# Kernel optimization log

Hardware: AMD Instinct MI355X
Metric: run time of the kernel (lower is better)

The kernel has to match this reference:

```python
import jax, jax.numpy as jnp
import numpy as np

T = 2048        # flattened tokens (one prefill sequence)
HID = 2048      # hidden_size
NH = 32         # query heads
NKV = 4         # kv heads
HD = 128        # head_dim
THETA = 1000000.0
EPS = 1e-6


def setup_inputs() -> dict:
    key = jax.random.key(0)
    k0, k1, k2 = jax.random.split(key, 3)
    return {
        "positions": jnp.arange(T, dtype=jnp.int32),
        "hidden_states": jax.random.normal(k0, (T, HID), dtype=jnp.float32),
        "w_qkv": jax.random.normal(k1, ((NH + 2 * NKV) * HD, HID), dtype=jnp.float32) * 0.02,
        "w_o": jax.random.normal(k2, (HID, NH * HD), dtype=jnp.float32) * 0.02,
        "q_norm_w": jnp.ones((HD,), dtype=jnp.float32),
        "k_norm_w": jnp.ones((HD,), dtype=jnp.float32),
    }


def _rmsnorm(x, w):
    # per-head RMSNorm over last dim (head_dim), fp32 math
    var = jnp.mean(x * x, axis=-1, keepdims=True)
    return x * jax.lax.rsqrt(var + EPS) * w


def _rope(x, positions):
    # NeoX-style rotary embedding over full head_dim
    d = x.shape[-1]
    inv_freq = 1.0 / (THETA ** (jnp.arange(0, d, 2, dtype=jnp.float32) / d))  # [d/2]
    ang = positions.astype(jnp.float32)[:, None] * inv_freq                   # [T, d/2]
    cos = jnp.cos(ang)[:, None, :]  # [T,1,d/2]
    sin = jnp.sin(ang)[:, None, :]
    x1, x2 = jnp.split(x, 2, axis=-1)
    return jnp.concatenate([x1 * cos - x2 * sin, x2 * cos + x1 * sin], axis=-1)


def reference(positions, hidden_states, w_qkv, w_o, q_norm_w, k_norm_w):
    # fused QKV projection (no bias)
    qkv = hidden_states @ w_qkv.T                       # [T, (NH+2*NKV)*HD]
    q, k, v = jnp.split(qkv, [NH * HD, (NH + NKV) * HD], axis=-1)
    q = _rmsnorm(q.reshape(T, NH, HD), q_norm_w)        # [T,NH,HD]
    k = _rmsnorm(k.reshape(T, NKV, HD), k_norm_w)       # [T,NKV,HD]
    v = v.reshape(T, NKV, HD)
    q = _rope(q, positions)
    k = _rope(k, positions)
    # GQA: expand kv heads to query heads
    g = NH // NKV
    k = jnp.repeat(k, g, axis=1)                        # [T,NH,HD]
    v = jnp.repeat(v, g, axis=1)
    scale = HD ** -0.5
    scores = jnp.einsum('qhd,khd->hqk', q, k) * scale   # [NH,T,T]
    causal = jnp.tril(jnp.ones((T, T), dtype=bool))
    scores = jnp.where(causal[None, :, :], scores, jnp.finfo(scores.dtype).min)
    attn = jax.nn.softmax(scores, axis=-1)
    o = jnp.einsum('hqk,khd->qhd', attn, v).reshape(T, NH * HD)
    return o @ w_o.T                                    # [T,HID]
```

## Files before the change

### kernel.cpp

```cpp
#include <hip/hip_runtime.h>
#include <math.h>

#define T 2048
#define HID 2048
#define NH 32
#define NKV 4
#define HD 128
#define QKV_DIM 5120
#define OD 4096
#define C2LOG 0.12751743f
#define MFIX 6.0f

typedef _Float16 half8 __attribute__((ext_vector_type(8)));
typedef _Float16 half4v __attribute__((ext_vector_type(4)));
typedef float floatx4 __attribute__((ext_vector_type(4)));

#define GLD16(gp, lp) __builtin_amdgcn_global_load_lds( \
    (const __attribute__((address_space(1))) void*)(gp), \
    (__attribute__((address_space(3))) void*)(lp), 16, 0, 0)

__global__ __launch_bounds__(256)
void cvt_all(const float* __restrict__ h, const float* __restrict__ wq,
             const float* __restrict__ wo, _Float16* __restrict__ out) {
    size_t i = ((size_t)blockIdx.x * 256 + threadIdx.x) * 4;
    const float* src;
    size_t off;
    if (i < (size_t)T * HID)                        { src = h;  off = i; }
    else if (i < (size_t)T * HID + (size_t)QKV_DIM * HID)
                                                    { src = wq; off = i - (size_t)T * HID; }
    else                                            { src = wo; off = i - (size_t)T * HID - (size_t)QKV_DIM * HID; }
    float4 v = *(const float4*)(src + off);
    half4v o = { (_Float16)v.x, (_Float16)v.y, (_Float16)v.z, (_Float16)v.w };
    *(half4v*)(out + i) = o;
}

__global__ __launch_bounds__(256)
void gemm_nt_h(const _Float16* __restrict__ A, const _Float16* __restrict__ B,
               _Float16* __restrict__ C, int M, int N, int K) {
    __shared__ __align__(16) _Float16 Asm[4096];
    __shared__ __align__(16) _Float16 Bsm[4096];
    int tid = threadIdx.x;
    int wave = tid >> 6, lane = tid & 63;
    int quad = lane >> 4, l16 = lane & 15;
    int m0 = blockIdx.y * 128, n0 = blockIdx.x * 128;
    int wm = (wave >> 1) * 64, wn = (wave & 1) * 64;
    const _Float16* Ag = A + (size_t)(m0 + (tid >> 2)) * K + (tid & 3) * 8;
    const _Float16* Bg = B + (size_t)(n0 + (tid >> 2)) * K + (tid & 3) * 8;
    size_t row64 = (size_t)64 * K;
    _Float16* AsmW = Asm + wave * 512;
    _Float16* BsmW = Bsm + wave * 512;
    floatx4 acc[4][4] = {};
    for (int k0 = 0; k0 < K; k0 += 32) {
        __syncthreads();
        GLD16(Ag + k0, AsmW);
        GLD16(Ag + row64 + k0, AsmW + 2048);
        GLD16(Bg + k0, BsmW);
        GLD16(Bg + row64 + k0, BsmW + 2048);
        __syncthreads();
        half8 af[4], bf[4];
        #pragma unroll
        for (int i = 0; i < 4; i++)
            af[i] = *(const half8*)&Asm[(wm + i * 16 + l16) * 32 + quad * 8];
        #pragma unroll
        for (int j = 0; j < 4; j++)
            bf[j] = *(const half8*)&Bsm[(wn + j * 16 + l16) * 32 + quad * 8];
        #pragma unroll
        for (int i = 0; i < 4; i++)
            #pragma unroll
            for (int j = 0; j < 4; j++)
                acc[i][j] = __builtin_amdgcn_mfma_f32_16x16x32_f16(af[i], bf[j], acc[i][j], 0, 0, 0);
    }
    #pragma unroll
    for (int i = 0; i < 4; i++) {
        int row = m0 + wm + i * 16 + quad * 4;
        #pragma unroll
        for (int j = 0; j < 4; j++) {
            int col = n0 + wn + j * 16 + l16;
            #pragma unroll
            for (int r = 0; r < 4; r++)
                C[(size_t)(row + r) * N + col] = (_Float16)acc[i][j][r];
        }
    }
}

__global__ __launch_bounds__(256)
void gemm_nt_64(const _Float16* __restrict__ A, const _Float16* __restrict__ B,
                float* __restrict__ C, int M, int N, int K) {
    __shared__ __align__(16) _Float16 Asm[4096];
    __shared__ __align__(16) _Float16 Bsm[2048];
    int tid = threadIdx.x;
    int wave = tid >> 6, lane = tid & 63;
    int quad = lane >> 4, l16 = lane & 15;
    int m0 = blockIdx.y * 128, n0 = blockIdx.x * 64;
    int wm = wave * 32;
    const _Float16* Ag = A + (size_t)(m0 + (tid >> 2)) * K + (tid & 3) * 8;
    const _Float16* Bg = B + (size_t)(n0 + (tid >> 2)) * K + (tid & 3) * 8;
    size_t row64 = (size_t)64 * K;
    _Float16* AsmW = Asm + wave * 512;
    _Float16* BsmW = Bsm + wave * 512;
    floatx4 acc[2][4] = {};
    for (int k0 = 0; k0 < K; k0 += 32) {
        __syncthreads();
        GLD16(Ag + k0, AsmW);
        GLD16(Ag + row64 + k0, AsmW + 2048);
        GLD16(Bg + k0, BsmW);
        __syncthreads();
        half8 af[2], bf[4];
        #pragma unroll
        for (int i = 0; i < 2; i++)
            af[i] = *(const half8*)&Asm[(wm + i * 16 + l16) * 32 + quad * 8];
        #pragma unroll
        for (int j = 0; j < 4; j++)
            bf[j] = *(const half8*)&Bsm[(j * 16 + l16) * 32 + quad * 8];
        #pragma unroll
        for (int i = 0; i < 2; i++)
            #pragma unroll
            for (int j = 0; j < 4; j++)
                acc[i][j] = __builtin_amdgcn_mfma_f32_16x16x32_f16(af[i], bf[j], acc[i][j], 0, 0, 0);
    }
    #pragma unroll
    for (int i = 0; i < 2; i++) {
        int row = m0 + wm + i * 16 + quad * 4;
        #pragma unroll
        for (int j = 0; j < 4; j++) {
            int col = n0 + j * 16 + l16;
            #pragma unroll
            for (int r = 0; r < 4; r++)
                C[(size_t)(row + r) * N + col] = acc[i][j][r];
        }
    }
}

__global__ __launch_bounds__(256)
void qkv_post(const _Float16* __restrict__ qkv, const int* __restrict__ positions,
              const float* __restrict__ qw, const float* __restrict__ kw,
              _Float16* __restrict__ Qb, _Float16* __restrict__ Kb,
              _Float16* __restrict__ Vt) {
    int t = blockIdx.x;
    int wave = threadIdx.x >> 6, lane = threadIdx.x & 63;
    float pos = (float)positions[t];
    float f = exp2f(-(float)lane * (19.9315685693241741f / 64.0f));
    float ang = pos * f;
    float s = sinf(ang), c = cosf(ang);
    const _Float16* row = qkv + (size_t)t * QKV_DIM;
    for (int hh = wave; hh < NH + 2 * NKV; hh += 4) {
        float x1 = (float)row[hh * HD + lane];
        float x2 = (float)row[hh * HD + lane + 64];
        if (hh < NH + NKV) {
            float ss = x1 * x1 + x2 * x2;
            for (int o = 1; o < 64; o <<= 1) ss += __shfl_xor(ss, o);
            float inv = rsqrtf(ss * (1.0f / HD) + 1e-6f);
            const float* w = (hh < NH) ? qw : kw;
            x1 = x1 * inv * w[lane];
            x2 = x2 * inv * w[lane + 64];
            float y1 = x1 * c - x2 * s;
            float y2 = x2 * c + x1 * s;
            _Float16* dst;
            if (hh < NH) dst = Qb + ((size_t)hh * T + t) * HD;
            else         dst = Kb + ((size_t)(hh - NH) * T + t) * HD;
            dst[lane]      = (_Float16)y1;
            dst[lane + 64] = (_Float16)y2;
        } else {
            int hk = hh - NH - NKV;
            Vt[((size_t)hk * HD + lane) * T + t]      = (_Float16)x1;
            Vt[((size_t)hk * HD + lane + 64) * T + t] = (_Float16)x2;
        }
    }
}

__global__ __launch_bounds__(256, 4)
void attn(const _Float16* __restrict__ Qb, const _Float16* __restrict__ Kb,
          const _Float16* __restrict__ Vt, _Float16* __restrict__ Ob) {
    __shared__ __align__(16) _Float16 Ksm[8192];
    __shared__ __align__(16) _Float16 Vsm[8192];
    __shared__ __align__(16) _Float16 Psm[4][1024];
    int b = blockIdx.x;
    int h = b & 31;
    int quarter = b >> 8;
    int i = (b & 255) >> 5;
    int qt = (quarter == 0) ? 31 - i : (quarter == 1) ? i
           : (quarter == 2) ? 23 - i : 8 + i;
    int hk = h >> 3;
    int tid = threadIdx.x, wave = tid >> 6, lane = tid & 63;
    int quad = lane >> 4, l16 = lane & 15;
    int q0 = qt * 64;
    int wbase = q0 + wave * 16;

    half8 aq[4];
    {
        const _Float16* qp = Qb + ((size_t)h * T + wbase + l16) * HD + quad * 8;
        #pragma unroll
        for (int dk = 0; dk < 4; dk++)
            aq[dk] = *(const half8*)(qp + dk * 32);
    }
    floatx4 o_acc[8] = {};
    float lpart[4] = {};

    int krow = tid >> 4;
    const _Float16* Kg = Kb + ((size_t)hk * T + krow) * HD + ((tid & 15) ^ (krow & 7)) * 8;
    int vrow = tid >> 3;
    const _Float16* Vg = Vt + ((size_t)hk * HD + vrow) * T + ((tid & 7) ^ (vrow & 7)) * 8;
    _Float16* KsmW = Ksm + wave * 512;
    _Float16* VsmW = Vsm + wave * 512;
    _Float16* PsmW = Psm[wave];

    int ntiles = qt + 1;
    for (int it = 0; it < ntiles; it++) {
        int kv0 = it * 64;
        __syncthreads();
        {
            const _Float16* kg = Kg + (size_t)kv0 * HD;
            const _Float16* vg = Vg + kv0;
            #pragma unroll
            for (int c = 0; c < 4; c++) {
                GLD16(kg + (size_t)c * (16 * HD), KsmW + c * 2048);
                GLD16(vg + (size_t)c * (32 * T), VsmW + c * 2048);
            }
        }
        __syncthreads();

        floatx4 sfr[4];
        #pragma unroll
        for (int sn = 0; sn < 4; sn++) {
            int row = sn * 16 + l16;
            int rs = row & 7;
            floatx4 a = {};
            #pragma unroll
            for (int dk = 0; dk < 4; dk++) {
                half8 kf = *(const half8*)&Ksm[row * 128 + ((dk * 4 + quad) ^ rs) * 8];
                a = __builtin_amdgcn_mfma_f32_16x16x32_f16(aq[dk], kf, a, 0, 0, 0);
            }
            sfr[sn] = a;
        }

        bool needmask = (it == ntiles - 1);
        int rq = wbase + quad * 4;
        #pragma unroll
        for (int sn = 0; sn < 4; sn++) {
            int kv = kv0 + sn * 16 + l16;
            #pragma unroll
            for (int r = 0; r < 4; r++) {
                float p = __builtin_amdgcn_exp2f(
                    __builtin_fmaf(sfr[sn][r], C2LOG, -MFIX));
                if (needmask) p = (kv <= rq + r) ? p : 0.0f;
                lpart[r] += p;
                int prow = quad * 4 + r;
                int cb = sn * 2 + (l16 >> 3);
                PsmW[prow * 64 + ((cb ^ (prow & 7)) * 8 + (l16 & 7))] = (_Float16)p;
            }
        }
        half8 ap0 = *(const half8*)&PsmW[l16 * 64 + ((quad ^ (l16 & 7)) * 8)];
        half8 ap1 = *(const half8*)&PsmW[l16 * 64 + (((4 + quad) ^ (l16 & 7)) * 8)];

        #pragma unroll
        for (int dn = 0; dn < 8; dn++) {
            int row = dn * 16 + l16;
            int rs = row & 7;
            half8 v0 = *(const half8*)&Vsm[row * 64 + ((quad ^ rs) * 8)];
            half8 v1 = *(const half8*)&Vsm[row * 64 + (((4 + quad) ^ rs) * 8)];
            o_acc[dn] = __builtin_amdgcn_mfma_f32_16x16x32_f16(ap0, v0, o_acc[dn], 0, 0, 0);
            o_acc[dn] = __builtin_amdgcn_mfma_f32_16x16x32_f16(ap1, v1, o_acc[dn], 0, 0, 0);
        }
    }

    #pragma unroll
    for (int o = 1; o < 16; o <<= 1)
        #pragma unroll
        for (int r = 0; r < 4; r++)
            lpart[r] += __shfl_xor(lpart[r], o);
    float linv[4];
    #pragma unroll
    for (int r = 0; r < 4; r++) linv[r] = 1.0f / lpart[r];
    int rowb = wbase + quad * 4;
    #pragma unroll
    for (int dn = 0; dn < 8; dn++) {
        int col = h * HD + dn * 16 + l16;
        #pragma unroll
        for (int r = 0; r < 4; r++)
            Ob[(size_t)(rowb + r) * OD + col] = (_Float16)(o_acc[dn][r] * linv[r]);
    }
}

extern "C" void kernel_launch(void* const* d_in, const int* in_sizes, int n_in,
                              void* d_out, int out_size, void* d_ws, size_t ws_size,
                              hipStream_t stream) {
    const int*   positions = (const int*)d_in[0];
    const float* hidden    = (const float*)d_in[1];
    const float* w_qkv     = (const float*)d_in[2];
    const float* w_o       = (const float*)d_in[3];
    const float* q_norm_w  = (const float*)d_in[4];
    const float* k_norm_w  = (const float*)d_in[5];
    float* out = (float*)d_out;

    char* ws = (char*)d_ws;
    _Float16* hb    = (_Float16*)(ws);
    _Float16* wqkvb = (_Float16*)(ws + 8388608);
    _Float16* wob   = (_Float16*)(ws + 29360128);
    _Float16* qkvh  = (_Float16*)(ws + 46137344);
    _Float16* Qb    = (_Float16*)(ws + 88080384);
    _Float16* Kb    = (_Float16*)(ws + 104857600);
    _Float16* Vt    = (_Float16*)(ws + 106954752);
    _Float16* Ob    = (_Float16*)(ws + 109051904);

    cvt_all<<<22528, 256, 0, stream>>>(hidden, w_qkv, w_o, hb);

    gemm_nt_h<<<dim3(QKV_DIM / 128, T / 128), 256, 0, stream>>>(hb, wqkvb, qkvh, T, QKV_DIM, HID);

    qkv_post<<<T, 256, 0, stream>>>(qkvh, positions, q_norm_w, k_norm_w, Qb, Kb, Vt);

    attn<<<1024, 256, 0, stream>>>(Qb, Kb, Vt, Ob);

    gemm_nt_64<<<dim3(HID / 64, T / 128), 256, 0, stream>>>(Ob, wob, out, T, HID, OD);
}
```

Baseline: 350.0 us.

## Split-K both projection GEMMs and fold the partial sums into consumers

The QKV GEMM now splits K into two halves across blockIdx.z and writes two fp16 partial buffers, which qkv_post sums on load. The output projection switches to 128x128 tiles with a 4-way K split into fp32 partials, followed by a new reduce4 kernel that adds them. The aim is more blocks per GEMM, for better CU occupancy and less tail imbalance. In exchange it adds partial-buffer memory traffic, an extra kernel launch, and some precision loss from storing fp16 partials. The partial buffers reuse workspace regions that are dead by then.

```diff
diff --git a/kernel.cpp b/kernel.cpp
--- a/kernel.cpp
+++ b/kernel.cpp
@@ -35,22 +35,25 @@
 }
 
 __global__ __launch_bounds__(256)
-void gemm_nt_h(const _Float16* __restrict__ A, const _Float16* __restrict__ B,
-               _Float16* __restrict__ C, int M, int N, int K) {
+void gemm_sk_h(const _Float16* __restrict__ A, const _Float16* __restrict__ B,
+               _Float16* __restrict__ p0, _Float16* __restrict__ p1,
+               int M, int N, int K, int KS) {
     __shared__ __align__(16) _Float16 Asm[4096];
     __shared__ __align__(16) _Float16 Bsm[4096];
     int tid = threadIdx.x;
     int wave = tid >> 6, lane = tid & 63;
     int quad = lane >> 4, l16 = lane & 15;
     int m0 = blockIdx.y * 128, n0 = blockIdx.x * 128;
+    int koff = blockIdx.z * KS;
+    _Float16* C = blockIdx.z ? p1 : p0;
     int wm = (wave >> 1) * 64, wn = (wave & 1) * 64;
-    const _Float16* Ag = A + (size_t)(m0 + (tid >> 2)) * K + (tid & 3) * 8;
-    const _Float16* Bg = B + (size_t)(n0 + (tid >> 2)) * K + (tid & 3) * 8;
+    const _Float16* Ag = A + (size_t)(m0 + (tid >> 2)) * K + koff + (tid & 3) * 8;
+    const _Float16* Bg = B + (size_t)(n0 + (tid >> 2)) * K + koff + (tid & 3) * 8;
     size_t row64 = (size_t)64 * K;
     _Float16* AsmW = Asm + wave * 512;
     _Float16* BsmW = Bsm + wave * 512;
     floatx4 acc[4][4] = {};
-    for (int k0 = 0; k0 < K; k0 += 32) {
+    for (int k0 = 0; k0 < KS; k0 += 32) {
         __syncthreads();
         GLD16(Ag + k0, AsmW);
         GLD16(Ag + row64 + k0, AsmW + 2048);
@@ -84,46 +87,52 @@
 }
 
 __global__ __launch_bounds__(256)
-void gemm_nt_64(const _Float16* __restrict__ A, const _Float16* __restrict__ B,
-                float* __restrict__ C, int M, int N, int K) {
+void gemm_sk_f(const _Float16* __restrict__ A, const _Float16* __restrict__ B,
+               float* __restrict__ p0, float* __restrict__ p1,
+               float* __restrict__ p2, float* __restrict__ p3,
+               int M, int N, int K, int KS) {
     __shared__ __align__(16) _Float16 Asm[4096];
-    __shared__ __align__(16) _Float16 Bsm[2048];
+    __shared__ __align__(16) _Float16 Bsm[4096];
     int tid = threadIdx.x;
     int wave = tid >> 6, lane = tid & 63;
     int quad = lane >> 4, l16 = lane & 15;
-    int m0 = blockIdx.y * 128, n0 = blockIdx.x * 64;
-    int wm = wave * 32;
-    const _Float16* Ag = A + (size_t)(m0 + (tid >> 2)) * K + (tid & 3) * 8;
-    const _Float16* Bg = B + (size_t)(n0 + (tid >> 2)) * K + (tid & 3) * 8;
+    int m0 = blockIdx.y * 128, n0 = blockIdx.x * 128;
+    int bz = blockIdx.z;
+    int koff = bz * KS;
+    float* C = (bz == 0) ? p0 : (bz == 1) ? p1 : (bz == 2) ? p2 : p3;
+    int wm = (wave >> 1) * 64, wn = (wave & 1) * 64;
+    const _Float16* Ag = A + (size_t)(m0 + (tid >> 2)) * K + koff + (tid & 3) * 8;
+    const _Float16* Bg = B + (size_t)(n0 + (tid >> 2)) * K + koff + (tid & 3) * 8;
     size_t row64 = (size_t)64 * K;
     _Float16* AsmW = Asm + wave * 512;
     _Float16* BsmW = Bsm + wave * 512;
-    floatx4 acc[2][4] = {};
-    for (int k0 = 0; k0 < K; k0 += 32) {
+    floatx4 acc[4][4] = {};
+    for (int k0 = 0; k0 < KS; k0 += 32) {
         __syncthreads();
         GLD16(Ag + k0, AsmW);
         GLD16(Ag + row64 + k0, AsmW + 2048);
         GLD16(Bg + k0, BsmW);
-        __syncthreads();
-        half8 af[2], bf[4];
-        #pragma unroll
-        for (int i = 0; i < 2; i++)
+        GLD16(Bg + row64 + k0, BsmW + 2048);
+        __syncthreads();
+        half8 af[4], bf[4];
+        #pragma unroll
+        for (int i = 0; i < 4; i++)
             af[i] = *(const half8*)&Asm[(wm + i * 16 + l16) * 32 + quad * 8];
         #pragma unroll
         for (int j = 0; j < 4; j++)
-            bf[j] = *(const half8*)&Bsm[(j * 16 + l16) * 32 + quad * 8];
-        #pragma unroll
-        for (int i = 0; i < 2; i++)
+            bf[j] = *(const half8*)&Bsm[(wn + j * 16 + l16) * 32 + quad * 8];
+        #pragma unroll
+        for (int i = 0; i < 4; i++)
             #pragma unroll
             for (int j = 0; j < 4; j++)
                 acc[i][j] = __builtin_amdgcn_mfma_f32_16x16x32_f16(af[i], bf[j], acc[i][j], 0, 0, 0);
     }
     #pragma unroll
-    for (int i = 0; i < 2; i++) {
+    for (int i = 0; i < 4; i++) {
         int row = m0 + wm + i * 16 + quad * 4;
         #pragma unroll
         for (int j = 0; j < 4; j++) {
-            int col = n0 + j * 16 + l16;
+            int col = n0 + wn + j * 16 + l16;
             #pragma unroll
             for (int r = 0; r < 4; r++)
                 C[(size_t)(row + r) * N + col] = acc[i][j][r];
@@ -132,7 +141,22 @@
 }
 
 __global__ __launch_bounds__(256)
-void qkv_post(const _Float16* __restrict__ qkv, const int* __restrict__ positions,
+void reduce4(const float* __restrict__ p0, const float* __restrict__ p1,
+             const float* __restrict__ p2, const float* __restrict__ p3,
+             float* __restrict__ out) {
+    size_t i = ((size_t)blockIdx.x * 256 + threadIdx.x) * 4;
+    float4 a = *(const float4*)(p0 + i);
+    float4 b = *(const float4*)(p1 + i);
+    float4 c = *(const float4*)(p2 + i);
+    float4 d = *(const float4*)(p3 + i);
+    float4 o = { a.x + b.x + c.x + d.x, a.y + b.y + c.y + d.y,
+                 a.z + b.z + c.z + d.z, a.w + b.w + c.w + d.w };
+    *(float4*)(out + i) = o;
+}
+
+__global__ __launch_bounds__(256)
+void qkv_post(const _Float16* __restrict__ qp0, const _Float16* __restrict__ qp1,
+              const int* __restrict__ positions,
               const float* __restrict__ qw, const float* __restrict__ kw,
               _Float16* __restrict__ Qb, _Float16* __restrict__ Kb,
               _Float16* __restrict__ Vt) {
@@ -142,10 +166,11 @@
     float f = exp2f(-(float)lane * (19.9315685693241741f / 64.0f));
     float ang = pos * f;
     float s = sinf(ang), c = cosf(ang);
-    const _Float16* row = qkv + (size_t)t * QKV_DIM;
+    const _Float16* r0 = qp0 + (size_t)t * QKV_DIM;
+    const _Float16* r1 = qp1 + (size_t)t * QKV_DIM;
     for (int hh = wave; hh < NH + 2 * NKV; hh += 4) {
-        float x1 = (float)row[hh * HD + lane];
-        float x2 = (float)row[hh * HD + lane + 64];
+        float x1 = (float)r0[hh * HD + lane] + (float)r1[hh * HD + lane];
+        float x2 = (float)r0[hh * HD + lane + 64] + (float)r1[hh * HD + lane + 64];
         if (hh < NH + NKV) {
             float ss = x1 * x1 + x2 * x2;
             for (int o = 1; o < 64; o <<= 1) ss += __shfl_xor(ss, o);
@@ -292,23 +317,32 @@
     const float* k_norm_w  = (const float*)d_in[5];
     float* out = (float*)d_out;
 
+    const size_t MiB = 1048576;
     char* ws = (char*)d_ws;
     _Float16* hb    = (_Float16*)(ws);
-    _Float16* wqkvb = (_Float16*)(ws + 8388608);
-    _Float16* wob   = (_Float16*)(ws + 29360128);
-    _Float16* qkvh  = (_Float16*)(ws + 46137344);
-    _Float16* Qb    = (_Float16*)(ws + 88080384);
-    _Float16* Kb    = (_Float16*)(ws + 104857600);
-    _Float16* Vt    = (_Float16*)(ws + 106954752);
-    _Float16* Ob    = (_Float16*)(ws + 109051904);
+    _Float16* wqkvb = (_Float16*)(ws + 8 * MiB);
+    _Float16* wob   = (_Float16*)(ws + 28 * MiB);
+    _Float16* qkvp0 = (_Float16*)(ws + 44 * MiB);
+    _Float16* qkvp1 = (_Float16*)(ws + 64 * MiB);
+    _Float16* Qb    = (_Float16*)(ws + 84 * MiB);
+    _Float16* Kb    = (_Float16*)(ws + 100 * MiB);
+    _Float16* Vt    = (_Float16*)(ws + 102 * MiB);
+    _Float16* Ob    = (_Float16*)(ws + 104 * MiB);
+    float*    op0   = (float*)(ws);
+    float*    op1   = (float*)(ws + 44 * MiB);
+    float*    op2   = (float*)(ws + 60 * MiB);
+    float*    op3   = (float*)(ws + 84 * MiB);
 
     cvt_all<<<22528, 256, 0, stream>>>(hidden, w_qkv, w_o, hb);
 
-    gemm_nt_h<<<dim3(QKV_DIM / 128, T / 128), 256, 0, stream>>>(hb, wqkvb, qkvh, T, QKV_DIM, HID);
-
-    qkv_post<<<T, 256, 0, stream>>>(qkvh, positions, q_norm_w, k_norm_w, Qb, Kb, Vt);
+    gemm_sk_h<<<dim3(QKV_DIM / 128, T / 128, 2), 256, 0, stream>>>(
+        hb, wqkvb, qkvp0, qkvp1, T, QKV_DIM, HID, HID / 2);
+
+    qkv_post<<<T, 256, 0, stream>>>(qkvp0, qkvp1, positions, q_norm_w, k_norm_w, Qb, Kb, Vt);
 
     attn<<<1024, 256, 0, stream>>>(Qb, Kb, Vt, Ob);
 
-    gemm_nt_64<<<dim3(HID / 64, T / 128), 256, 0, stream>>>(Ob, wob, out, T, HID, OD);
-}
+    gemm_sk_f<<<dim3(HID / 128, T / 128, 4), 256, 0, stream>>>(
+        Ob, wob, op0, op1, op2, op3, T, HID, OD, OD / 4);
+    reduce4<<<T * HID / 1024, 256, 0, stream>>>(op0, op1, op2, op3, out);
+}
```

Result: faster. 343.0 us (-2.0%).
